# Optimization experiments

Measured on AMD Instinct MI355X. Metric: run time of the kernel, lower is better.

Reference implementation:

```python
import jax, jax.numpy as jnp
import numpy as np

WS = 7          # window_size
N = WS * WS     # 49 tokens per window
DIM = 384
H = 12
HD = DIM // H   # 32
NW = 64         # windows per image (mask leading dim)


def _rel_pos_index():
    coords = np.stack(np.meshgrid(np.arange(WS), np.arange(WS), indexing='ij'))  # (2, WS, WS)
    cf = coords.reshape(2, -1)                      # (2, N)
    rel = cf[:, :, None] - cf[:, None, :]           # (2, N, N)
    rel = rel.transpose(1, 2, 0)                    # (N, N, 2)
    idx = (rel[..., 0] + WS - 1) * (2 * WS - 1) + (rel[..., 1] + WS - 1)
    return jnp.asarray(idx, dtype=jnp.int32)        # (N, N)

REL_IDX = _rel_pos_index()


def setup_inputs() -> dict:
    key = jax.random.key(0)
    ks = jax.random.split(key, 10)
    B_ = 2048
    x = jax.random.normal(ks[0], (B_, N, DIM), dtype=jnp.float32)
    mask = jnp.zeros((NW, N, N), dtype=jnp.float32)
    s = 0.02
    Wq = jax.random.normal(ks[1], (DIM, DIM), jnp.float32) * s
    Wk = jax.random.normal(ks[2], (DIM, DIM), jnp.float32) * s
    Wv = jax.random.normal(ks[3], (DIM, DIM), jnp.float32) * s
    Wp = jax.random.normal(ks[4], (DIM, DIM), jnp.float32) * s
    bq = jnp.zeros((DIM,), jnp.float32)
    bk = jnp.zeros((DIM,), jnp.float32)
    bv = jnp.zeros((DIM,), jnp.float32)
    bp = jnp.zeros((DIM,), jnp.float32)
    table = jax.random.normal(ks[5], ((2 * WS - 1) ** 2, H), jnp.float32) * s
    return {"x": x, "mask": mask, "Wq": Wq, "bq": bq, "Wk": Wk, "bk": bk,
            "Wv": Wv, "bv": bv, "Wp": Wp, "bp": bp, "table": table}


def reference(x, mask, Wq, bq, Wk, bk, Wv, bv, Wp, bp, table):
    b_, n, c = x.shape
    scale = HD ** (-0.5)
    # projections: PyTorch Linear is x @ W.T + b
    q = (x @ Wq.T + bq).reshape(b_, n, H, HD).transpose(0, 2, 1, 3)  # (B, H, N, D)
    k = (x @ Wk.T + bk).reshape(b_, n, H, HD).transpose(0, 2, 1, 3)
    v = (x @ Wv.T + bv).reshape(b_, n, H, HD).transpose(0, 2, 1, 3)
    attn = jnp.einsum('bhnd,bhmd->bhnm', q * scale, k)               # (B, H, N, N)
    rel_bias = table[REL_IDX]                                        # (N, N, H)
    attn = attn + rel_bias.transpose(2, 0, 1)[None]                  # broadcast over B
    # mask add: (B//nW, nW, H, N, N) + mask[None, :, None]
    nw = mask.shape[0]
    attn = attn.reshape(b_ // nw, nw, H, n, n) + mask[None, :, None]
    attn = attn.reshape(b_, H, n, n)
    attn = jax.nn.softmax(attn, axis=-1)
    out = jnp.einsum('bhnm,bhmd->bhnd', attn, v)                     # (B, H, N, D)
    out = out.transpose(0, 2, 1, 3).reshape(b_, n, c)
    return out @ Wp.T + bp
```

## Files before the change

kernel.cpp:

```cpp
#include <hip/hip_runtime.h>
#include <stdint.h>

using bf16x8 = __attribute__((ext_vector_type(8))) short;
using f32x4  = __attribute__((ext_vector_type(4))) float;

__device__ __forceinline__ short f2bf(float f) {
  uint32_t u = __float_as_uint(f);
  u += 0x7fff + ((u >> 16) & 1u);
  return (short)(u >> 16);
}

#define MFMA16(a, b, c) __builtin_amdgcn_mfma_f32_16x16x32_bf16((a), (b), (c), 0, 0, 0)

__device__ __forceinline__ void gl_lds16(const short* g, short* l) {
  __builtin_amdgcn_global_load_lds(
      (const __attribute__((address_space(1))) void*)g,
      (__attribute__((address_space(3))) void*)l, 16, 0, 0);
}

__global__ void prep_w(const float* __restrict__ Wq, const float* __restrict__ bq,
                       const float* __restrict__ Wk, const float* __restrict__ bk,
                       const float* __restrict__ Wv, const float* __restrict__ bv,
                       const float* __restrict__ Wp, const float* __restrict__ bp,
                       short* __restrict__ Wqkv, short* __restrict__ Wpb,
                       float* __restrict__ bqkv, float* __restrict__ bpb) {
  int i = blockIdx.x * 256 + threadIdx.x;
  const float scale = 0.17677669529663687f;
  if (i < 1152 * 384) {
    int r = i / 384, k = i - r * 384;
    float v;
    if (r < 384)      v = Wq[r * 384 + k] * scale;
    else if (r < 768) v = Wk[(r - 384) * 384 + k];
    else              v = Wv[(r - 768) * 384 + k];
    Wqkv[i] = f2bf(v);
  }
  if (i < 384 * 384) Wpb[i] = f2bf(Wp[i]);
  if (i < 1152) bqkv[i] = (i < 384) ? bq[i] * scale : ((i < 768) ? bk[i - 384] : bv[i - 768]);
  if (i < 384) bpb[i] = bp[i];
}

__global__ void prep_bm(const float* __restrict__ table, const float* __restrict__ mask,
                        float* __restrict__ bm, int nwmask) {
  int wm = blockIdx.x / 12, h = blockIdx.x - wm * 12;
  const float* mrow = mask + (size_t)wm * 2401;
  float* dst = bm + (size_t)blockIdx.x * 2401;
  for (int e = threadIdx.x; e < 2401; e += 256) {
    int i = e / 49, j = e - i * 49;
    int id = i / 7, ir = i - id * 7;
    int jd = j / 7, jr = j - jd * 7;
    int idx = (id - jd + 6) * 13 + (ir - jr + 6);
    dst[e] = table[idx * 12 + h] + mrow[e];
  }
}

__global__ void prep_x(const float* __restrict__ x, short* __restrict__ xb, int n8) {
  int u = blockIdx.x * 256 + threadIdx.x;
  if (u < n8) {
    int e = u * 8;
    float4 f0 = *(const float4*)(x + e);
    float4 f1 = *(const float4*)(x + e + 4);
    bf16x8 cv;
    cv[0] = f2bf(f0.x); cv[1] = f2bf(f0.y); cv[2] = f2bf(f0.z); cv[3] = f2bf(f0.w);
    cv[4] = f2bf(f1.x); cv[5] = f2bf(f1.y); cv[6] = f2bf(f1.z); cv[7] = f2bf(f1.w);
    *(bf16x8*)(xb + e) = cv;
  }
}

__global__ __launch_bounds__(256) void qkv_gemm(
    const short* __restrict__ xb, const short* __restrict__ Wqkv,
    const float* __restrict__ bqkv,
    short* __restrict__ qws, short* __restrict__ kws, short* __restrict__ vws,
    int ntok) {
  __shared__ __align__(16) short smem[2 * 320 * 64];
  const int tid = threadIdx.x;
  const int lane = tid & 63, wv = tid >> 6;
  const int c = lane & 15, g = lane >> 4;

  const int mt = gridDim.y;
  int id = blockIdx.y * 6 + blockIdx.x;
  int mt8 = mt & ~7;
  int xq, yq;
  if (id < 6 * mt8) {
    int q = id / 48, r = id - q * 48;
    yq = q * 8 + (r & 7);
    xq = r >> 3;
  } else {
    int rem = id - 6 * mt8;
    xq = rem % 6;
    yq = mt8 + rem / 6;
  }
  const int n0 = xq * 192;
  const int row0 = yq * 128;

  f32x4 acc[8][3];
  const f32x4 zero = {0.f, 0.f, 0.f, 0.f};
#pragma unroll
  for (int m = 0; m < 8; m++)
#pragma unroll
    for (int nn = 0; nn < 3; nn++) acc[m][nn] = zero;

  const int rsub = lane >> 3;
  const int chnk = ((lane & 7) ^ rsub) * 8;
  const short* aS[4];
  const short* bS[6];
#pragma unroll
  for (int i = 0; i < 4; i++) {
    int r = (wv * 4 + i) * 8 + rsub;
    int grow = row0 + r;
    if (grow >= ntok) grow = ntok - 1;
    aS[i] = xb + (size_t)grow * 384 + chnk;
  }
#pragma unroll
  for (int j = 0; j < 6; j++) {
    int r = (wv * 6 + j) * 8 + rsub;
    bS[j] = Wqkv + (size_t)(n0 + r) * 384 + chnk;
  }

  auto stage = [&](int buf, int ks) {
    short* Asl = smem + buf * (320 * 64);
    short* Bsl = Asl + 128 * 64;
#pragma unroll
    for (int i = 0; i < 4; i++)
      gl_lds16(aS[i] + ks * 64, Asl + (wv * 4 + i) * 512);
#pragma unroll
    for (int j = 0; j < 6; j++)
      gl_lds16(bS[j] + ks * 64, Bsl + (wv * 6 + j) * 512);
  };

  stage(0, 0);
  __syncthreads();
  for (int ks = 0; ks < 6; ks++) {
    const int cur = ks & 1;
    if (ks < 5) stage(cur ^ 1, ks + 1);
    const short* Asl = smem + cur * (320 * 64);
    const short* Bsl = Asl + 128 * 64;
#pragma unroll
    for (int kk = 0; kk < 2; kk++) {
      bf16x8 af[8];
#pragma unroll
      for (int m = 0; m < 8; m++) {
        int row = m * 16 + c;
        af[m] = *(const bf16x8*)&Asl[row * 64 + (((kk * 4 + g) ^ (row & 7)) * 8)];
      }
#pragma unroll
      for (int nn = 0; nn < 3; nn++) {
        int row = wv * 48 + nn * 16 + c;
        bf16x8 bfr = *(const bf16x8*)&Bsl[row * 64 + (((kk * 4 + g) ^ (row & 7)) * 8)];
#pragma unroll
        for (int m = 0; m < 8; m++) acc[m][nn] = MFMA16(af[m], bfr, acc[m][nn]);
      }
    }
    __syncthreads();
  }

  const int s = n0 / 384;
  short* base = (s == 0) ? qws : ((s == 1) ? kws : vws);
  const int hbase = (n0 - s * 384) >> 5;
#pragma unroll
  for (int half = 0; half < 2; half++) {
    __syncthreads();
#pragma unroll
    for (int nn = 0; nn < 3; nn++) {
      int colRel = wv * 48 + nn * 16 + c;
      float bias = bqkv[n0 + colRel];
#pragma unroll
      for (int mm = 0; mm < 4; mm++) {
        int m = half * 4 + mm;
#pragma unroll
        for (int r = 0; r < 4; r++)
          smem[(mm * 16 + g * 4 + r) * 200 + colRel] = f2bf(acc[m][nn][r] + bias);
      }
    }
    __syncthreads();
    for (int u = tid; u < 384; u += 256) {
      int row = u & 63, j = u >> 6;
      int tr = row0 + half * 64 + row;
      if (tr < ntok) {
        int bw = tr / 49;
        int n = tr - bw * 49;
        short* dst = base + ((size_t)(bw * 12 + hbase + j) * 49 + n) * 32;
        const uint4* src = (const uint4*)&smem[row * 200 + j * 32];
        uint4* d4 = (uint4*)dst;
        d4[0] = src[0]; d4[1] = src[1]; d4[2] = src[2]; d4[3] = src[3];
      }
    }
  }
}

__global__ __launch_bounds__(256) void attn_kernel(
    const short* __restrict__ qws, const short* __restrict__ kws,
    const short* __restrict__ vws, short* __restrict__ ows,
    const float* __restrict__ bm, int b0, int nwmask) {
  __shared__ short Pall[4 * 64 * 72];
  const int tid = threadIdx.x;
  const int lane = tid & 63, wvi = tid >> 6;
  const int c = lane & 15, g = lane >> 4;
  const int task = blockIdx.x * 4 + wvi;
  const int b = task / 12, h = task - b * 12;
  const int wm = (b0 + b) % nwmask;
  const short* qb = qws + (size_t)(b * 12 + h) * 1568;
  const short* kb = kws + (size_t)(b * 12 + h) * 1568;
  const short* vb = vws + (size_t)(b * 12 + h) * 1568;

  bf16x8 qf[4], kf[4];
#pragma unroll
  for (int m = 0; m < 4; m++) { int i = m * 16 + c; if (i > 48) i = 48; qf[m] = *(const bf16x8*)(qb + i * 32 + g * 8); }
#pragma unroll
  for (int n = 0; n < 4; n++) { int j = n * 16 + c; if (j > 48) j = 48; kf[n] = *(const bf16x8*)(kb + j * 32 + g * 8); }

  const f32x4 zero = {0.f, 0.f, 0.f, 0.f};
  f32x4 S[4][4];
#pragma unroll
  for (int m = 0; m < 4; m++)
#pragma unroll
    for (int n = 0; n < 4; n++) S[m][n] = MFMA16(qf[m], kf[n], zero);

  const float* bmh = bm + (size_t)(wm * 12 + h) * 2401;
#pragma unroll
  for (int n = 0; n < 4; n++) {
    int j = n * 16 + c;
    if (j < 49) {
#pragma unroll
      for (int m = 0; m < 4; m++)
#pragma unroll
        for (int r = 0; r < 4; r++) {
          int i = m * 16 + g * 4 + r; if (i > 48) i = 48;
          S[m][n][r] += bmh[i * 49 + j];
        }
    } else {
#pragma unroll
      for (int m = 0; m < 4; m++)
#pragma unroll
        for (int r = 0; r < 4; r++) S[m][n][r] = -3.0e38f;
    }
  }

  short* P = Pall + wvi * 4608;
#pragma unroll
  for (int m = 0; m < 4; m++)
#pragma unroll
    for (int r = 0; r < 4; r++) {
      float mx = fmaxf(fmaxf(S[m][0][r], S[m][1][r]), fmaxf(S[m][2][r], S[m][3][r]));
      mx = fmaxf(mx, __shfl_xor(mx, 1));
      mx = fmaxf(mx, __shfl_xor(mx, 2));
      mx = fmaxf(mx, __shfl_xor(mx, 4));
      mx = fmaxf(mx, __shfl_xor(mx, 8));
      float e0 = __expf(S[m][0][r] - mx);
      float e1 = __expf(S[m][1][r] - mx);
      float e2 = __expf(S[m][2][r] - mx);
      float e3 = __expf(S[m][3][r] - mx);
      float sm = (e0 + e1) + (e2 + e3);
      sm += __shfl_xor(sm, 1);
      sm += __shfl_xor(sm, 2);
      sm += __shfl_xor(sm, 4);
      sm += __shfl_xor(sm, 8);
      float rinv = 1.0f / sm;
      int row = m * 16 + g * 4 + r;
      P[row * 72 + c]      = f2bf(e0 * rinv);
      P[row * 72 + 16 + c] = f2bf(e1 * rinv);
      P[row * 72 + 32 + c] = f2bf(e2 * rinv);
      P[row * 72 + 48 + c] = f2bf(e3 * rinv);
    }

  f32x4 O[4][2];
#pragma unroll
  for (int m = 0; m < 4; m++) { O[m][0] = zero; O[m][1] = zero; }
#pragma unroll
  for (int kk = 0; kk < 2; kk++) {
    bf16x8 pf[4];
#pragma unroll
    for (int m = 0; m < 4; m++) pf[m] = *(const bf16x8*)&P[(m * 16 + c) * 72 + kk * 32 + g * 8];
#pragma unroll
    for (int dt = 0; dt < 2; dt++) {
      bf16x8 vf;
#pragma unroll
      for (int rr = 0; rr < 8; rr++) {
        int j = kk * 32 + g * 8 + rr; if (j > 48) j = 48;
        vf[rr] = vb[j * 32 + dt * 16 + c];
      }
#pragma unroll
      for (int m = 0; m < 4; m++) O[m][dt] = MFMA16(pf[m], vf, O[m][dt]);
    }
  }
#pragma unroll
  for (int m = 0; m < 4; m++)
#pragma unroll
    for (int r = 0; r < 4; r++) {
      int i = m * 16 + g * 4 + r;
      if (i < 49) {
        size_t o = ((size_t)b * 49 + i) * 384 + h * 32;
        ows[o + c]      = f2bf(O[m][0][r]);
        ows[o + 16 + c] = f2bf(O[m][1][r]);
      }
    }
}

__global__ __launch_bounds__(256) void proj_gemm(
    const short* __restrict__ ows, const short* __restrict__ Wpb,
    const float* __restrict__ bpb, float* __restrict__ out,
    long tok0, int ntok) {
  __shared__ __align__(16) short smem[2 * 320 * 64];
  const int tid = threadIdx.x;
  const int lane = tid & 63, wv = tid >> 6;
  const int c = lane & 15, g = lane >> 4;

  const int mt = gridDim.y;
  int id = blockIdx.y * 2 + blockIdx.x;
  int mt8 = mt & ~7;
  int xq, yq;
  if (id < 2 * mt8) {
    int q = id / 16, r = id - q * 16;
    yq = q * 8 + (r & 7);
    xq = r >> 3;
  } else {
    int rem = id - 2 * mt8;
    xq = rem % 2;
    yq = mt8 + rem / 2;
  }
  const int n0 = xq * 192;
  const int row0 = yq * 128;

  f32x4 acc[8][3];
  const f32x4 zero = {0.f, 0.f, 0.f, 0.f};
#pragma unroll
  for (int m = 0; m < 8; m++)
#pragma unroll
    for (int nn = 0; nn < 3; nn++) acc[m][nn] = zero;

  const int rsub = lane >> 3;
  const int chnk = ((lane & 7) ^ rsub) * 8;
  const short* aS[4];
  const short* bS[6];
#pragma unroll
  for (int i = 0; i < 4; i++) {
    int r = (wv * 4 + i) * 8 + rsub;
    int grow = row0 + r;
    if (grow >= ntok) grow = ntok - 1;
    aS[i] = ows + (size_t)grow * 384 + chnk;
  }
#pragma unroll
  for (int j = 0; j < 6; j++) {
    int r = (wv * 6 + j) * 8 + rsub;
    bS[j] = Wpb + (size_t)(n0 + r) * 384 + chnk;
  }

  auto stage = [&](int buf, int ks) {
    short* Asl = smem + buf * (320 * 64);
    short* Bsl = Asl + 128 * 64;
#pragma unroll
    for (int i = 0; i < 4; i++)
      gl_lds16(aS[i] + ks * 64, Asl + (wv * 4 + i) * 512);
#pragma unroll
    for (int j = 0; j < 6; j++)
      gl_lds16(bS[j] + ks * 64, Bsl + (wv * 6 + j) * 512);
  };

  stage(0, 0);
  __syncthreads();
  for (int ks = 0; ks < 6; ks++) {
    const int cur = ks & 1;
    if (ks < 5) stage(cur ^ 1, ks + 1);
    const short* Asl = smem + cur * (320 * 64);
    const short* Bsl = Asl + 128 * 64;
#pragma unroll
    for (int kk = 0; kk < 2; kk++) {
      bf16x8 af[8];
#pragma unroll
      for (int m = 0; m < 8; m++) {
        int row = m * 16 + c;
        af[m] = *(const bf16x8*)&Asl[row * 64 + (((kk * 4 + g) ^ (row & 7)) * 8)];
      }
#pragma unroll
      for (int nn = 0; nn < 3; nn++) {
        int row = wv * 48 + nn * 16 + c;
        bf16x8 bfr = *(const bf16x8*)&Bsl[row * 64 + (((kk * 4 + g) ^ (row & 7)) * 8)];
#pragma unroll
        for (int m = 0; m < 8; m++) acc[m][nn] = MFMA16(af[m], bfr, acc[m][nn]);
      }
    }
    __syncthreads();
  }
#pragma unroll
  for (int nn = 0; nn < 3; nn++) {
    int cg = n0 + wv * 48 + nn * 16 + c;
    float bias = bpb[cg];
#pragma unroll
    for (int m = 0; m < 8; m++)
#pragma unroll
      for (int r = 0; r < 4; r++) {
        int tr = row0 + m * 16 + g * 4 + r;
        if (tr < ntok) out[((size_t)(tok0 + tr)) * 384 + cg] = acc[m][nn][r] + bias;
      }
  }
}

extern "C" void kernel_launch(void* const* d_in, const int* in_sizes, int n_in,
                              void* d_out, int out_size, void* d_ws, size_t ws_size,
                              hipStream_t stream) {
  const float* x    = (const float*)d_in[0];
  const float* mask = (const float*)d_in[1];
  const float* Wq = (const float*)d_in[2];
  const float* bq = (const float*)d_in[3];
  const float* Wk = (const float*)d_in[4];
  const float* bk = (const float*)d_in[5];
  const float* Wv = (const float*)d_in[6];
  const float* bv = (const float*)d_in[7];
  const float* Wp = (const float*)d_in[8];
  const float* bp = (const float*)d_in[9];
  const float* table = (const float*)d_in[10];
  float* out = (float*)d_out;

  const int Btot = in_sizes[0] / (49 * 384);
  const int NWm  = in_sizes[1] / (49 * 49);

  char* ws = (char*)d_ws;
  short* Wqkv = (short*)ws;
  short* Wpb  = Wqkv + 1152 * 384;
  float* bqkv = (float*)(Wpb + 384 * 384);
  float* bpb  = bqkv + 1152;
  float* bmp  = bpb + 384;
  size_t fixedB = (size_t)(1152 * 384 + 384 * 384) * 2 + (1152 + 384) * 4
                + (size_t)NWm * 12 * 2401 * 4;
  char* dyn = ws + ((fixedB + 255) & ~(size_t)255);
  size_t used = (size_t)(dyn - ws);
  size_t avail = (ws_size > used + 4096) ? (ws_size - used - 4096) : 0;
  const size_t perw = (size_t)5 * 18816 * 2;
  long nwc = (long)(avail / perw);
  if (nwc > Btot) nwc = Btot;
  if (nwc >= 64) nwc &= ~63L;
  if (nwc < 1) nwc = 1;
  short* xbw = (short*)dyn;
  short* qws = xbw + (size_t)nwc * 18816;
  short* kws = qws + (size_t)nwc * 18816;
  short* vws = kws + (size_t)nwc * 18816;
  short* ows = vws + (size_t)nwc * 18816;

  prep_w<<<dim3(1728), dim3(256), 0, stream>>>(Wq, bq, Wk, bk, Wv, bv, Wp, bp,
                                               Wqkv, Wpb, bqkv, bpb);
  prep_bm<<<dim3(NWm * 12), dim3(256), 0, stream>>>(table, mask, bmp, NWm);

  for (long b0 = 0; b0 < Btot; b0 += nwc) {
    int nw = (int)((Btot - b0 < nwc) ? (Btot - b0) : nwc);
    int ntok = nw * 49;
    long tok0 = b0 * 49;
    int n8 = ntok * 48;
    prep_x<<<dim3((n8 + 255) / 256), dim3(256), 0, stream>>>(x + tok0 * 384, xbw, n8);
    int mt = (ntok + 127) / 128;
    qkv_gemm<<<dim3(6, mt), dim3(256), 0, stream>>>(xbw, Wqkv, bqkv, qws, kws, vws, ntok);
    attn_kernel<<<dim3(3 * nw), dim3(256), 0, stream>>>(qws, kws, vws, ows, bmp,
                                                        (int)b0, NWm);
    proj_gemm<<<dim3(2, mt), dim3(256), 0, stream>>>(ows, Wpb, bpb, out, tok0, ntok);
  }
}
```

Before: 624.0 us.

## Store V transposed and padded so attention loads V fragments as vectors

```diff
diff --git a/kernel.cpp b/kernel.cpp
--- a/kernel.cpp
+++ b/kernel.cpp
@@ -154,34 +154,67 @@
   }
 
   const int s = n0 / 384;
-  short* base = (s == 0) ? qws : ((s == 1) ? kws : vws);
   const int hbase = (n0 - s * 384) >> 5;
-#pragma unroll
-  for (int half = 0; half < 2; half++) {
-    __syncthreads();
-#pragma unroll
-    for (int nn = 0; nn < 3; nn++) {
-      int colRel = wv * 48 + nn * 16 + c;
-      float bias = bqkv[n0 + colRel];
-#pragma unroll
-      for (int mm = 0; mm < 4; mm++) {
-        int m = half * 4 + mm;
-#pragma unroll
-        for (int r = 0; r < 4; r++)
-          smem[(mm * 16 + g * 4 + r) * 200 + colRel] = f2bf(acc[m][nn][r] + bias);
-      }
-    }
-    __syncthreads();
-    for (int u = tid; u < 384; u += 256) {
-      int row = u & 63, j = u >> 6;
+  if (s < 2) {
+    short* base = (s == 0) ? qws : kws;
+#pragma unroll
+    for (int half = 0; half < 2; half++) {
+      __syncthreads();
+#pragma unroll
+      for (int nn = 0; nn < 3; nn++) {
+        int colRel = wv * 48 + nn * 16 + c;
+        float bias = bqkv[n0 + colRel];
+#pragma unroll
+        for (int mm = 0; mm < 4; mm++) {
+          int m = half * 4 + mm;
+#pragma unroll
+          for (int r = 0; r < 4; r++)
+            smem[(mm * 16 + g * 4 + r) * 200 + colRel] = f2bf(acc[m][nn][r] + bias);
+        }
+      }
+      __syncthreads();
+      for (int u = tid; u < 384; u += 256) {
+        int row = u & 63, j = u >> 6;
+        int tr = row0 + half * 64 + row;
+        if (tr < ntok) {
+          int bw = tr / 49;
+          int n = tr - bw * 49;
+          short* dst = base + ((size_t)(bw * 12 + hbase + j) * 49 + n) * 32;
+          const uint4* src = (const uint4*)&smem[row * 200 + j * 32];
+          uint4* d4 = (uint4*)dst;
+          d4[0] = src[0]; d4[1] = src[1]; d4[2] = src[2]; d4[3] = src[3];
+        }
+      }
+    }
+  } else {
+#pragma unroll
+    for (int half = 0; half < 2; half++) {
+      __syncthreads();
+#pragma unroll
+      for (int nn = 0; nn < 3; nn++) {
+        int colRel = wv * 48 + nn * 16 + c;
+        float bias = bqkv[n0 + colRel];
+#pragma unroll
+        for (int mm = 0; mm < 4; mm++) {
+          int m = half * 4 + mm;
+#pragma unroll
+          for (int r = 0; r < 4; r++)
+            smem[(mm * 16 + g * 4 + r) * 194 + colRel] = f2bf(acc[m][nn][r] + bias);
+        }
+      }
+      __syncthreads();
+      int row = tid & 63;
       int tr = row0 + half * 64 + row;
       if (tr < ntok) {
         int bw = tr / 49;
         int n = tr - bw * 49;
-        short* dst = base + ((size_t)(bw * 12 + hbase + j) * 49 + n) * 32;
-        const uint4* src = (const uint4*)&smem[row * 200 + j * 32];
-        uint4* d4 = (uint4*)dst;
-        d4[0] = src[0]; d4[1] = src[1]; d4[2] = src[2]; d4[3] = src[3];
+        short* wbase = vws + ((size_t)(bw * 12 + hbase) * 32) * 64 + n;
+        const short* srow = &smem[row * 194];
+#pragma unroll 4
+        for (int it = 0; it < 48; it++) {
+          int col = (tid >> 6) * 48 + it;
+          wbase[(size_t)col * 64] = srow[col];
+        }
       }
     }
   }
@@ -200,13 +233,25 @@
   const int wm = (b0 + b) % nwmask;
   const short* qb = qws + (size_t)(b * 12 + h) * 1568;
   const short* kb = kws + (size_t)(b * 12 + h) * 1568;
-  const short* vb = vws + (size_t)(b * 12 + h) * 1568;
+  const short* vtb = vws + (size_t)(b * 12 + h) * 2048;
 
   bf16x8 qf[4], kf[4];
 #pragma unroll
   for (int m = 0; m < 4; m++) { int i = m * 16 + c; if (i > 48) i = 48; qf[m] = *(const bf16x8*)(qb + i * 32 + g * 8); }
 #pragma unroll
   for (int n = 0; n < 4; n++) { int j = n * 16 + c; if (j > 48) j = 48; kf[n] = *(const bf16x8*)(kb + j * 32 + g * 8); }
+
+  bf16x8 vfr[2][2];
+#pragma unroll
+  for (int kk = 0; kk < 2; kk++)
+#pragma unroll
+    for (int dt = 0; dt < 2; dt++)
+      vfr[kk][dt] = *(const bf16x8*)(vtb + (dt * 16 + c) * 64 + kk * 32 + g * 8);
+#pragma unroll
+  for (int dt = 0; dt < 2; dt++)
+#pragma unroll
+    for (int rr = 0; rr < 8; rr++)
+      if (g * 8 + rr > 16) vfr[1][dt][rr] = 0;
 
   const f32x4 zero = {0.f, 0.f, 0.f, 0.f};
   f32x4 S[4][4];
@@ -271,16 +316,9 @@
 #pragma unroll
     for (int m = 0; m < 4; m++) pf[m] = *(const bf16x8*)&P[(m * 16 + c) * 72 + kk * 32 + g * 8];
 #pragma unroll
-    for (int dt = 0; dt < 2; dt++) {
-      bf16x8 vf;
-#pragma unroll
-      for (int rr = 0; rr < 8; rr++) {
-        int j = kk * 32 + g * 8 + rr; if (j > 48) j = 48;
-        vf[rr] = vb[j * 32 + dt * 16 + c];
-      }
-#pragma unroll
-      for (int m = 0; m < 4; m++) O[m][dt] = MFMA16(pf[m], vf, O[m][dt]);
-    }
+    for (int dt = 0; dt < 2; dt++)
+#pragma unroll
+      for (int m = 0; m < 4; m++) O[m][dt] = MFMA16(pf[m], vfr[kk][dt], O[m][dt]);
   }
 #pragma unroll
   for (int m = 0; m < 4; m++)
@@ -424,7 +462,7 @@
   char* dyn = ws + ((fixedB + 255) & ~(size_t)255);
   size_t used = (size_t)(dyn - ws);
   size_t avail = (ws_size > used + 4096) ? (ws_size - used - 4096) : 0;
-  const size_t perw = (size_t)5 * 18816 * 2;
+  const size_t perw = (size_t)(4 * 18816 + 24576) * 2;
   long nwc = (long)(avail / perw);
   if (nwc > Btot) nwc = Btot;
   if (nwc >= 64) nwc &= ~63L;
@@ -433,7 +471,7 @@
   short* qws = xbw + (size_t)nwc * 18816;
   short* kws = qws + (size_t)nwc * 18816;
   short* vws = kws + (size_t)nwc * 18816;
-  short* ows = vws + (size_t)nwc * 18816;
+  short* ows = vws + (size_t)nwc * 24576;
 
   prep_w<<<dim3(1728), dim3(256), 0, stream>>>(Wq, bq, Wk, bk, Wv, bv, Wp, bp,
                                                Wqkv, Wpb, bqkv, bpb);
```

Result: slower. 664.3 us (+6.5%).

## Pre-tile bias/mask into MFMA fragment layout, hoist V loads, defer softmax normalization

Applied to the files above, without the earlier changes.

```diff
diff --git a/kernel.cpp b/kernel.cpp
--- a/kernel.cpp
+++ b/kernel.cpp
@@ -40,16 +40,21 @@
 }
 
 __global__ void prep_bm(const float* __restrict__ table, const float* __restrict__ mask,
-                        float* __restrict__ bm, int nwmask) {
+                        float* __restrict__ bmL, int nwmask) {
   int wm = blockIdx.x / 12, h = blockIdx.x - wm * 12;
   const float* mrow = mask + (size_t)wm * 2401;
-  float* dst = bm + (size_t)blockIdx.x * 2401;
-  for (int e = threadIdx.x; e < 2401; e += 256) {
-    int i = e / 49, j = e - i * 49;
-    int id = i / 7, ir = i - id * 7;
-    int jd = j / 7, jr = j - jd * 7;
-    int idx = (id - jd + 6) * 13 + (ir - jr + 6);
-    dst[e] = table[idx * 12 + h] + mrow[e];
+  float* dst = bmL + (size_t)blockIdx.x * 4096;
+  for (int e = threadIdx.x; e < 4096; e += 256) {
+    int mn = e >> 8, c = (e >> 4) & 15, i = e & 15;
+    int row = (mn >> 2) * 16 + i, col = (mn & 3) * 16 + c;
+    float v = -3.0e38f;
+    if (row < 49 && col < 49) {
+      int id = row / 7, ir = row - id * 7;
+      int jd = col / 7, jr = col - jd * 7;
+      int idx = (id - jd + 6) * 13 + (ir - jr + 6);
+      v = table[idx * 12 + h] + mrow[row * 49 + col];
+    }
+    dst[e] = v;
   }
 }
 
@@ -208,6 +213,20 @@
 #pragma unroll
   for (int n = 0; n < 4; n++) { int j = n * 16 + c; if (j > 48) j = 48; kf[n] = *(const bf16x8*)(kb + j * 32 + g * 8); }
 
+  bf16x8 vfr[2][2];
+#pragma unroll
+  for (int kk = 0; kk < 2; kk++)
+#pragma unroll
+    for (int dt = 0; dt < 2; dt++) {
+      bf16x8 vf;
+#pragma unroll
+      for (int rr = 0; rr < 8; rr++) {
+        int j = kk * 32 + g * 8 + rr; if (j > 48) j = 48;
+        vf[rr] = vb[j * 32 + dt * 16 + c];
+      }
+      vfr[kk][dt] = vf;
+    }
+
   const f32x4 zero = {0.f, 0.f, 0.f, 0.f};
   f32x4 S[4][4];
 #pragma unroll
@@ -215,26 +234,17 @@
 #pragma unroll
     for (int n = 0; n < 4; n++) S[m][n] = MFMA16(qf[m], kf[n], zero);
 
-  const float* bmh = bm + (size_t)(wm * 12 + h) * 2401;
-#pragma unroll
-  for (int n = 0; n < 4; n++) {
-    int j = n * 16 + c;
-    if (j < 49) {
-#pragma unroll
-      for (int m = 0; m < 4; m++)
-#pragma unroll
-        for (int r = 0; r < 4; r++) {
-          int i = m * 16 + g * 4 + r; if (i > 48) i = 48;
-          S[m][n][r] += bmh[i * 49 + j];
-        }
-    } else {
-#pragma unroll
-      for (int m = 0; m < 4; m++)
-#pragma unroll
-        for (int r = 0; r < 4; r++) S[m][n][r] = -3.0e38f;
-    }
-  }
-
+  const float* bmh = bm + (size_t)(wm * 12 + h) * 4096;
+#pragma unroll
+  for (int m = 0; m < 4; m++)
+#pragma unroll
+    for (int n = 0; n < 4; n++) {
+      f32x4 b4 = *(const f32x4*)(bmh + ((m * 4 + n) * 16 + c) * 16 + g * 4);
+      S[m][n][0] += b4[0]; S[m][n][1] += b4[1];
+      S[m][n][2] += b4[2]; S[m][n][3] += b4[3];
+    }
+
+  float rv[4][4];
   short* P = Pall + wvi * 4608;
 #pragma unroll
   for (int m = 0; m < 4; m++)
@@ -254,12 +264,12 @@
       sm += __shfl_xor(sm, 2);
       sm += __shfl_xor(sm, 4);
       sm += __shfl_xor(sm, 8);
-      float rinv = 1.0f / sm;
+      rv[m][r] = 1.0f / sm;
       int row = m * 16 + g * 4 + r;
-      P[row * 72 + c]      = f2bf(e0 * rinv);
-      P[row * 72 + 16 + c] = f2bf(e1 * rinv);
-      P[row * 72 + 32 + c] = f2bf(e2 * rinv);
-      P[row * 72 + 48 + c] = f2bf(e3 * rinv);
+      P[row * 72 + c]      = f2bf(e0);
+      P[row * 72 + 16 + c] = f2bf(e1);
+      P[row * 72 + 32 + c] = f2bf(e2);
+      P[row * 72 + 48 + c] = f2bf(e3);
     }
 
   f32x4 O[4][2];
@@ -271,16 +281,9 @@
 #pragma unroll
     for (int m = 0; m < 4; m++) pf[m] = *(const bf16x8*)&P[(m * 16 + c) * 72 + kk * 32 + g * 8];
 #pragma unroll
-    for (int dt = 0; dt < 2; dt++) {
-      bf16x8 vf;
-#pragma unroll
-      for (int rr = 0; rr < 8; rr++) {
-        int j = kk * 32 + g * 8 + rr; if (j > 48) j = 48;
-        vf[rr] = vb[j * 32 + dt * 16 + c];
-      }
-#pragma unroll
-      for (int m = 0; m < 4; m++) O[m][dt] = MFMA16(pf[m], vf, O[m][dt]);
-    }
+    for (int dt = 0; dt < 2; dt++)
+#pragma unroll
+      for (int m = 0; m < 4; m++) O[m][dt] = MFMA16(pf[m], vfr[kk][dt], O[m][dt]);
   }
 #pragma unroll
   for (int m = 0; m < 4; m++)
@@ -289,8 +292,8 @@
       int i = m * 16 + g * 4 + r;
       if (i < 49) {
         size_t o = ((size_t)b * 49 + i) * 384 + h * 32;
-        ows[o + c]      = f2bf(O[m][0][r]);
-        ows[o + 16 + c] = f2bf(O[m][1][r]);
+        ows[o + c]      = f2bf(O[m][0][r] * rv[m][r]);
+        ows[o + 16 + c] = f2bf(O[m][1][r] * rv[m][r]);
       }
     }
 }
@@ -420,7 +423,7 @@
   float* bpb  = bqkv + 1152;
   float* bmp  = bpb + 384;
   size_t fixedB = (size_t)(1152 * 384 + 384 * 384) * 2 + (1152 + 384) * 4
-                + (size_t)NWm * 12 * 2401 * 4;
+                + (size_t)NWm * 12 * 4096 * 4;
   char* dyn = ws + ((fixedB + 255) & ~(size_t)255);
   size_t used = (size_t)(dyn - ws);
   size_t avail = (ws_size > used + 4096) ? (ws_size - used - 4096) : 0;
```

Result: faster. 600.7 us (-3.7%).
